# Kernel optimization log

Hardware: AMD Instinct MI355X
Metric: run time of the kernel (lower is better)

The kernel has to match this reference:

```python
import jax, jax.numpy as jnp
import numpy as np

B, S, D = 1, 2048, 2048
H, KVH, HD = 32, 8, 64  # heads, kv heads, head_dim
GROUPS = H // KVH
SCALE = HD ** -0.5


def rotate_half(x):
    x1, x2 = jnp.split(x, 2, axis=-1)
    return jnp.concatenate((-x2, x1), axis=-1)


def setup_inputs() -> dict:
    key = jax.random.key(0)
    ks = jax.random.split(key, 8)
    hidden_states = jax.random.normal(ks[0], (B, S, D), dtype=jnp.float32)
    # RoPE tables: [B, S, HD]
    inv_freq = 1.0 / (10000.0 ** (jnp.arange(0, HD, 2, dtype=jnp.float32) / HD))
    t = jnp.arange(S, dtype=jnp.float32)
    freqs = jnp.outer(t, inv_freq)                      # [S, HD/2]
    emb = jnp.concatenate((freqs, freqs), axis=-1)      # [S, HD]
    cos = jnp.cos(emb)[None]                            # [1, S, HD]
    sin = jnp.sin(emb)[None]
    std = 0.02
    wq = jax.random.normal(ks[1], (H * HD, D), dtype=jnp.float32) * std
    wk = jax.random.normal(ks[2], (KVH * HD, D), dtype=jnp.float32) * std
    wv = jax.random.normal(ks[3], (KVH * HD, D), dtype=jnp.float32) * std
    wo = jax.random.normal(ks[4], (D, H * HD), dtype=jnp.float32) * std
    return {"hidden_states": hidden_states, "cos": cos, "sin": sin,
            "wq": wq, "wk": wk, "wv": wv, "wo": wo}


def reference(hidden_states, cos, sin, wq, wk, wv, wo):
    b, s, d = hidden_states.shape
    # QKV projections (nn.Linear: x @ W.T), split into heads -> [B, H, S, HD]
    q = (hidden_states @ wq.T).reshape(b, s, H, HD).transpose(0, 2, 1, 3)
    k = (hidden_states @ wk.T).reshape(b, s, KVH, HD).transpose(0, 2, 1, 3)
    v = (hidden_states @ wv.T).reshape(b, s, KVH, HD).transpose(0, 2, 1, 3)
    # RoPE (unsqueeze_dim=1)
    c = cos[:, None, :, :]
    sn = sin[:, None, :, :]
    q = q * c + rotate_half(q) * sn
    k = k * c + rotate_half(k) * sn
    # GQA: repeat kv heads to match query heads
    k = jnp.repeat(k, GROUPS, axis=1)
    v = jnp.repeat(v, GROUPS, axis=1)
    # scaled causal softmax attention
    scores = jnp.einsum('bhqd,bhkd->bhqk', q, k) * SCALE
    causal = jnp.tril(jnp.ones((s, s), dtype=bool))
    scores = jnp.where(causal, scores, jnp.finfo(scores.dtype).min)
    probs = jax.nn.softmax(scores, axis=-1)
    attn = jnp.einsum('bhqk,bhkd->bhqd', probs, v)
    attn = attn.transpose(0, 2, 1, 3).reshape(b, s, H * HD)
    return attn @ wo.T
```

## Files before the change

### kernel.cpp

```cpp
#include <hip/hip_runtime.h>
#include <stdint.h>

#define SEQ   2048
#define DMODEL 2048
#define NQH   32
#define NKVH  8
#define HDIM  64
#define QN    (NQH*HDIM)
#define KVNN  (NKVH*HDIM)

typedef __bf16 bf16x8 __attribute__((ext_vector_type(8)));
typedef float  f32x4  __attribute__((ext_vector_type(4)));
typedef unsigned short u16;

__device__ __forceinline__ u16 f2bf(float f) {
  __bf16 h = (__bf16)f;
  return __builtin_bit_cast(u16, h);
}
__device__ __forceinline__ float bf2f(u16 b) {
  return __builtin_bit_cast(float, (uint32_t)b << 16);
}
__device__ __forceinline__ float fexp2(float x) {
#if __has_builtin(__builtin_amdgcn_exp2f)
  return __builtin_amdgcn_exp2f(x);
#else
  return __expf(0.69314718056f * x);
#endif
}
__device__ __forceinline__ bool probe_is_f32(const uint32_t* p) {
  return (p[0] & 0xFFFFu) == 0u;
}

__device__ __forceinline__ void glds16(const u16* g, void* lds) {
  __builtin_amdgcn_global_load_lds(
      (const __attribute__((address_space(1))) uint32_t*)g,
      (__attribute__((address_space(3))) uint32_t*)lds, 16, 0, 0);
}
__device__ __forceinline__ void drain_vm() {
  asm volatile("s_waitcnt vmcnt(0)" ::: "memory");
}

__global__ __launch_bounds__(256)
void conv_all(const void* __restrict__ X, const void* __restrict__ cosv,
              const void* __restrict__ sinv, const void* __restrict__ wq,
              const void* __restrict__ wk, const void* __restrict__ wv,
              const void* __restrict__ wo,
              u16* __restrict__ Xc, u16* __restrict__ cosc, u16* __restrict__ sinc,
              u16* __restrict__ wqc, u16* __restrict__ wkc, u16* __restrict__ wvc,
              u16* __restrict__ woc)
{
  const bool f32in = probe_is_f32((const uint32_t*)cosv);
  const long t = (long)blockIdx.x * 256 + threadIdx.x;
  const void* src; u16* dst; long off;
  if      (t < 524288L)  { src = X;    dst = Xc;   off = t; }
  else if (t < 1048576L) { src = wq;   dst = wqc;  off = t - 524288L; }
  else if (t < 1179648L) { src = wk;   dst = wkc;  off = t - 1048576L; }
  else if (t < 1310720L) { src = wv;   dst = wvc;  off = t - 1179648L; }
  else if (t < 1835008L) { src = wo;   dst = woc;  off = t - 1310720L; }
  else if (t < 1851392L) { src = cosv; dst = cosc; off = t - 1835008L; }
  else                   { src = sinv; dst = sinc; off = t - 1851392L; }
  if (f32in) {
    const float4* s = (const float4*)src;
    float4 a = s[2*off], b = s[2*off + 1];
    union { u16 h[8]; uint4 u; } o;
    o.h[0]=f2bf(a.x); o.h[1]=f2bf(a.y); o.h[2]=f2bf(a.z); o.h[3]=f2bf(a.w);
    o.h[4]=f2bf(b.x); o.h[5]=f2bf(b.y); o.h[6]=f2bf(b.z); o.h[7]=f2bf(b.w);
    *(uint4*)(dst + off*8) = o.u;
  } else {
    *(uint4*)(dst + off*8) = ((const uint4*)src)[off];
  }
}

__global__ __launch_bounds__(256, 4)
void gemm_qkv(const u16* __restrict__ A,
              const u16* __restrict__ wq, const u16* __restrict__ wk,
              const u16* __restrict__ wv,
              u16* __restrict__ Qb, u16* __restrict__ Kb, u16* __restrict__ Vb)
{
  __shared__ __align__(16) u16 As[2][64][32];
  __shared__ __align__(16) u16 Bs[2][128][32];
  const int tid  = threadIdx.x;
  const int wave = tid >> 6;
  const int lane = tid & 63;
  const int quad = lane >> 4;
  const int l16  = lane & 15;
  const int m0 = blockIdx.y * 64;
  const int n0 = blockIdx.x * 128;
  const int wm = (wave & 1) * 32;
  const int wn = (wave >> 1) * 64;
  const int K = DMODEL;
  const int lr = lane >> 2;
  const int lc = (lane & 3) * 8;

  const u16* Bbase; u16* Cbase; int Cstride, nc0;
  if (n0 < 2048)      { Bbase = wq + (size_t)n0 * K;          Cbase = Qb; Cstride = QN;   nc0 = n0; }
  else if (n0 < 2560) { Bbase = wk + (size_t)(n0 - 2048) * K; Cbase = Kb; Cstride = KVNN; nc0 = n0 - 2048; }
  else                { Bbase = wv + (size_t)(n0 - 2560) * K; Cbase = Vb; Cstride = KVNN; nc0 = n0 - 2560; }

  f32x4 acc[2][4];
  #pragma unroll
  for (int i = 0; i < 2; i++)
    #pragma unroll
    for (int j = 0; j < 4; j++)
      acc[i][j] = (f32x4){0.f, 0.f, 0.f, 0.f};

  #define STAGE_QKV(b, k0)                                                        \
    do {                                                                          \
      glds16(A + (size_t)(m0 + 16*wave + lr) * K + (k0) + lc,                     \
             (char*)&As[b][0][0] + wave*1024);                                    \
      glds16(Bbase + (size_t)(16*wave + lr) * K + (k0) + lc,                      \
             (char*)&Bs[b][0][0] + wave*1024);                                    \
      glds16(Bbase + (size_t)(64 + 16*wave + lr) * K + (k0) + lc,                 \
             (char*)&Bs[b][0][0] + (4+wave)*1024);                                \
    } while (0)

  STAGE_QKV(0, 0);
  drain_vm();
  __syncthreads();
  int cur = 0;
  for (int k0 = 0; k0 < K; k0 += 32) {
    if (k0 + 32 < K) STAGE_QKV(cur ^ 1, k0 + 32);
    bf16x8 af[2], bfr[4];
    #pragma unroll
    for (int i = 0; i < 2; i++) af[i]  = *(const bf16x8*)&As[cur][wm + i*16 + l16][quad*8];
    #pragma unroll
    for (int j = 0; j < 4; j++) bfr[j] = *(const bf16x8*)&Bs[cur][wn + j*16 + l16][quad*8];
    #pragma unroll
    for (int i = 0; i < 2; i++)
      #pragma unroll
      for (int j = 0; j < 4; j++)
        acc[i][j] = __builtin_amdgcn_mfma_f32_16x16x32_bf16(af[i], bfr[j], acc[i][j], 0, 0, 0);
    drain_vm();
    __syncthreads();
    cur ^= 1;
  }
  #undef STAGE_QKV

  #pragma unroll
  for (int i = 0; i < 2; i++) {
    const int rb = m0 + wm + i*16 + quad*4;
    #pragma unroll
    for (int j = 0; j < 4; j++) {
      const int col = nc0 + wn + j*16 + l16;
      #pragma unroll
      for (int r = 0; r < 4; r++)
        Cbase[(size_t)(rb + r) * Cstride + col] = f2bf(acc[i][j][r]);
    }
  }
}

__global__ __launch_bounds__(256, 4)
void gemm_nt(const u16* __restrict__ A, const u16* __restrict__ B,
             void* __restrict__ C, int M, int N, int K,
             const uint32_t* outprobe)
{
  __shared__ __align__(16) u16 As[2][64][32];
  __shared__ __align__(16) u16 Bs[2][128][32];
  const int tid  = threadIdx.x;
  const int wave = tid >> 6;
  const int lane = tid & 63;
  const int quad = lane >> 4;
  const int l16  = lane & 15;
  const int m0 = blockIdx.y * 64;
  const int n0 = blockIdx.x * 128;
  const int wm = (wave & 1) * 32;
  const int wn = (wave >> 1) * 64;
  const int lr = lane >> 2;
  const int lc = (lane & 3) * 8;

  f32x4 acc[2][4];
  #pragma unroll
  for (int i = 0; i < 2; i++)
    #pragma unroll
    for (int j = 0; j < 4; j++)
      acc[i][j] = (f32x4){0.f, 0.f, 0.f, 0.f};

  #define STAGE_NT(b, k0)                                                         \
    do {                                                                          \
      glds16(A + (size_t)(m0 + 16*wave + lr) * K + (k0) + lc,                     \
             (char*)&As[b][0][0] + wave*1024);                                    \
      glds16(B + (size_t)(n0 + 16*wave + lr) * K + (k0) + lc,                     \
             (char*)&Bs[b][0][0] + wave*1024);                                    \
      glds16(B + (size_t)(n0 + 64 + 16*wave + lr) * K + (k0) + lc,                \
             (char*)&Bs[b][0][0] + (4+wave)*1024);                                \
    } while (0)

  STAGE_NT(0, 0);
  drain_vm();
  __syncthreads();
  int cur = 0;
  for (int k0 = 0; k0 < K; k0 += 32) {
    if (k0 + 32 < K) STAGE_NT(cur ^ 1, k0 + 32);
    bf16x8 af[2], bfr[4];
    #pragma unroll
    for (int i = 0; i < 2; i++) af[i]  = *(const bf16x8*)&As[cur][wm + i*16 + l16][quad*8];
    #pragma unroll
    for (int j = 0; j < 4; j++) bfr[j] = *(const bf16x8*)&Bs[cur][wn + j*16 + l16][quad*8];
    #pragma unroll
    for (int i = 0; i < 2; i++)
      #pragma unroll
      for (int j = 0; j < 4; j++)
        acc[i][j] = __builtin_amdgcn_mfma_f32_16x16x32_bf16(af[i], bfr[j], acc[i][j], 0, 0, 0);
    drain_vm();
    __syncthreads();
    cur ^= 1;
  }
  #undef STAGE_NT

  const bool f32out = (outprobe != nullptr) && probe_is_f32(outprobe);
  #pragma unroll
  for (int i = 0; i < 2; i++) {
    const int rb = m0 + wm + i*16 + quad*4;
    #pragma unroll
    for (int j = 0; j < 4; j++) {
      const int col = n0 + wn + j*16 + l16;
      if (f32out) {
        float* Cf = (float*)C;
        #pragma unroll
        for (int r = 0; r < 4; r++)
          Cf[(size_t)(rb + r) * N + col] = acc[i][j][r];
      } else {
        u16* Ch = (u16*)C;
        #pragma unroll
        for (int r = 0; r < 4; r++)
          Ch[(size_t)(rb + r) * N + col] = f2bf(acc[i][j][r]);
      }
    }
  }
}

__global__ void rope_k(u16* __restrict__ Kb,
                       const u16* __restrict__ cosb, const u16* __restrict__ sinb)
{
  const int idx = blockIdx.x * 256 + threadIdx.x;
  const int s = idx >> 8;
  const int rem = idx & 255;
  u16* base = Kb + (size_t)s * KVNN + (rem >> 5) * 64;
  const int d = rem & 31;
  const float x1 = bf2f(base[d]);
  const float x2 = bf2f(base[d + 32]);
  const float c  = bf2f(cosb[s * 64 + d]);
  const float sn = bf2f(sinb[s * 64 + d]);
  base[d]      = f2bf(x1 * c - x2 * sn);
  base[d + 32] = f2bf(x2 * c + x1 * sn);
}

__global__ __launch_bounds__(256)
void vtrans(const u16* __restrict__ Vb, u16* __restrict__ Vtg)
{
  __shared__ __align__(16) u16 T[64][72];
  const int tid = threadIdx.x;
  const int hkv = blockIdx.x & 7;
  const int s0  = (blockIdx.x >> 3) * 64;
  const int r = tid >> 3;
  const int c = (tid & 7) * 8;
  *(uint4*)&T[r][c]      = *(const uint4*)(Vb + (size_t)(s0 + r)      * KVNN + hkv*64 + c);
  *(uint4*)&T[r + 32][c] = *(const uint4*)(Vb + (size_t)(s0 + r + 32) * KVNN + hkv*64 + c);
  __syncthreads();
  #pragma unroll
  for (int dd = 0; dd < 64; dd += 32) {
    const int d = (tid >> 3) + dd;
    union { u16 h[8]; uint4 u; } o;
    #pragma unroll
    for (int j = 0; j < 8; j++) o.h[j] = T[c + j][d];
    *(uint4*)(Vtg + (size_t)(hkv*64 + d) * SEQ + s0 + c) = o.u;
  }
}

#define LOG2E 1.4426950408889634f

__device__ __forceinline__ float qmax16(float v) {
  v = fmaxf(v, __shfl_xor(v, 1)); v = fmaxf(v, __shfl_xor(v, 2));
  v = fmaxf(v, __shfl_xor(v, 4)); v = fmaxf(v, __shfl_xor(v, 8));
  return v;
}
__device__ __forceinline__ float qsum16(float v) {
  v += __shfl_xor(v, 1); v += __shfl_xor(v, 2);
  v += __shfl_xor(v, 4); v += __shfl_xor(v, 8);
  return v;
}

__global__ __launch_bounds__(256, 4)
void attn_kernel(const u16* __restrict__ Qb,
                 const u16* __restrict__ Kb,
                 const u16* __restrict__ Vtg,
                 u16* __restrict__ Ob,
                 const u16* __restrict__ cosb, const u16* __restrict__ sinb)
{
  __shared__ __align__(16) u16 Ks[64][72];
  __shared__ __align__(16) u16 Vt[64][72];
  __shared__ __align__(16) u16 Ps[4][16][72];

  const int tid  = threadIdx.x;
  const int wave = tid >> 6;
  const int lane = tid & 63;
  const int quad = lane >> 4;
  const int l16  = lane & 15;
  const int h    = blockIdx.x;
  const int qt   = 31 - blockIdx.y;
  const int hkv  = h >> 2;
  const int qrow0 = qt * 64 + wave * 16;
  const int ktmax = qt + 1;

  bf16x8 qf[2];
  {
    const int qrow = qrow0 + l16;
    const u16* qp = Qb + (size_t)qrow * QN + h*64 + quad*8;
    union { bf16x8 v; u16 h8[8]; } lo, hi, cv, sv, olo, ohi;
    lo.v = *(const bf16x8*)qp;
    hi.v = *(const bf16x8*)(qp + 32);
    cv.v = *(const bf16x8*)(cosb + qrow*64 + quad*8);
    sv.v = *(const bf16x8*)(sinb + qrow*64 + quad*8);
    #pragma unroll
    for (int j = 0; j < 8; j++) {
      const float x1 = bf2f(lo.h8[j]), x2 = bf2f(hi.h8[j]);
      const float c = bf2f(cv.h8[j]), sn = bf2f(sv.h8[j]);
      olo.h8[j] = f2bf((x1*c - x2*sn) * 0.125f);
      ohi.h8[j] = f2bf((x2*c + x1*sn) * 0.125f);
    }
    qf[0] = olo.v;
    qf[1] = ohi.v;
  }

  f32x4 oacc[4];
  #pragma unroll
  for (int nt = 0; nt < 4; nt++) oacc[nt] = (f32x4){0.f, 0.f, 0.f, 0.f};
  float m_run[4], l_run[4];
  #pragma unroll
  for (int r = 0; r < 4; r++) { m_run[r] = -1e30f; l_run[r] = 0.f; }

  const int sr = tid >> 3;
  const int sc = (tid & 7) * 8;

  uint4 k0, k1, v0, v1;
  {
    k0 = *(const uint4*)(Kb + (size_t)(sr)      * KVNN + hkv*64 + sc);
    k1 = *(const uint4*)(Kb + (size_t)(sr + 32) * KVNN + hkv*64 + sc);
    v0 = *(const uint4*)(Vtg + (size_t)(hkv*64 + sr)      * SEQ + sc);
    v1 = *(const uint4*)(Vtg + (size_t)(hkv*64 + sr + 32) * SEQ + sc);
  }

  for (int kt = 0; kt < ktmax; kt++) {
    const int kb = kt * 64;
    const bool diag = (kt == qt);

    __syncthreads();
    *(uint4*)&Ks[sr][sc]      = k0;
    *(uint4*)&Ks[sr + 32][sc] = k1;
    *(uint4*)&Vt[sr][sc]      = v0;
    *(uint4*)&Vt[sr + 32][sc] = v1;
    __syncthreads();

    if (kt + 1 < ktmax) {
      const int kn = kb + 64;
      k0 = *(const uint4*)(Kb + (size_t)(kn + sr)      * KVNN + hkv*64 + sc);
      k1 = *(const uint4*)(Kb + (size_t)(kn + sr + 32) * KVNN + hkv*64 + sc);
      v0 = *(const uint4*)(Vtg + (size_t)(hkv*64 + sr)      * SEQ + kn + sc);
      v1 = *(const uint4*)(Vtg + (size_t)(hkv*64 + sr + 32) * SEQ + kn + sc);
    }

    f32x4 sacc[4];
    #pragma unroll
    for (int nt = 0; nt < 4; nt++) sacc[nt] = (f32x4){0.f, 0.f, 0.f, 0.f};
    #pragma unroll
    for (int ks = 0; ks < 2; ks++)
      #pragma unroll
      for (int nt = 0; nt < 4; nt++)
        if (!diag || nt <= wave) {
          bf16x8 kf = *(const bf16x8*)&Ks[nt*16 + l16][ks*32 + quad*8];
          sacc[nt] = __builtin_amdgcn_mfma_f32_16x16x32_bf16(qf[ks], kf, sacc[nt], 0, 0, 0);
        }
    #pragma unroll
    for (int nt = 0; nt < 4; nt++)
      #pragma unroll
      for (int r = 0; r < 4; r++)
        sacc[nt][r] *= LOG2E;
    if (diag) {
      #pragma unroll
      for (int nt = 0; nt < 4; nt++)
        #pragma unroll
        for (int r = 0; r < 4; r++)
          if (kb + nt*16 + l16 > qrow0 + quad*4 + r)
            sacc[nt][r] = -1e30f;
    }
    float alpha[4];
    #pragma unroll
    for (int r = 0; r < 4; r++) {
      float mx = fmaxf(fmaxf(sacc[0][r], sacc[1][r]), fmaxf(sacc[2][r], sacc[3][r]));
      mx = qmax16(mx);
      const float mnew = fmaxf(m_run[r], mx);
      alpha[r] = fexp2(m_run[r] - mnew);
      m_run[r] = mnew;
      float rs = 0.f;
      #pragma unroll
      for (int nt = 0; nt < 4; nt++) {
        const float p = fexp2(sacc[nt][r] - mnew);
        rs += p;
        Ps[wave][quad*4 + r][nt*16 + l16] = f2bf(p);
      }
      rs = qsum16(rs);
      l_run[r] = l_run[r] * alpha[r] + rs;
    }
    #pragma unroll
    for (int nt = 0; nt < 4; nt++)
      #pragma unroll
      for (int r = 0; r < 4; r++)
        oacc[nt][r] *= alpha[r];
    asm volatile("" ::: "memory");
    #pragma unroll
    for (int ks = 0; ks < 2; ks++) {
      if (diag && wave < 2 && ks == 1) continue;
      bf16x8 pf = *(const bf16x8*)&Ps[wave][l16][ks*32 + quad*8];
      #pragma unroll
      for (int nt = 0; nt < 4; nt++) {
        bf16x8 vf = *(const bf16x8*)&Vt[nt*16 + l16][ks*32 + quad*8];
        oacc[nt] = __builtin_amdgcn_mfma_f32_16x16x32_bf16(pf, vf, oacc[nt], 0, 0, 0);
      }
    }
  }

  #pragma unroll
  for (int r = 0; r < 4; r++) {
    const float inv = 1.0f / l_run[r];
    const int qrow = qrow0 + quad*4 + r;
    #pragma unroll
    for (int nt = 0; nt < 4; nt++)
      Ob[(size_t)qrow * QN + h*64 + nt*16 + l16] = f2bf(oacc[nt][r] * inv);
  }
}

extern "C" void kernel_launch(void* const* d_in, const int* in_sizes, int n_in,
                              void* d_out, int out_size, void* d_ws, size_t ws_size,
                              hipStream_t stream) {
  const void* X    = d_in[0];
  const void* cosr = d_in[1];
  const void* sinr = d_in[2];
  const void* wq   = d_in[3];
  const void* wk   = d_in[4];
  const void* wv   = d_in[5];
  const void* wo   = d_in[6];

  char* ws = (char*)d_ws;
  const size_t MB = 1024u * 1024u;
  u16* Xc   = (u16*)(ws);
  u16* wqc  = (u16*)(ws + 8*MB);
  u16* wkc  = (u16*)(ws + 16*MB);
  u16* wvc  = (u16*)(ws + 18*MB);
  u16* woc  = (u16*)(ws + 20*MB);
  u16* cosc = (u16*)(ws + 28*MB);
  u16* sinc = (u16*)(ws + 28*MB + 256*1024);
  u16* Qb   = (u16*)(ws + 28*MB + 512*1024);
  u16* Kb   = (u16*)(ws + 36*MB + 512*1024);
  u16* Vb   = (u16*)(ws + 38*MB + 512*1024);
  u16* Vtg  = (u16*)(ws + 40*MB + 512*1024);
  u16* Ab   = wqc;

  dim3 blk(256);
  conv_all<<<dim3(7296), blk, 0, stream>>>(X, cosr, sinr, wq, wk, wv, wo,
                                           Xc, cosc, sinc, wqc, wkc, wvc, woc);
  gemm_qkv<<<dim3(24, 32), blk, 0, stream>>>(Xc, wqc, wkc, wvc, Qb, Kb, Vb);
  rope_k<<<dim3((SEQ*NKVH*32)/256), blk, 0, stream>>>(Kb, cosc, sinc);
  vtrans<<<dim3(256), blk, 0, stream>>>(Vb, Vtg);
  attn_kernel<<<dim3(NQH, SEQ/64), blk, 0, stream>>>(Qb, Kb, Vtg, Ab, cosc, sinc);
  gemm_nt<<<dim3(16, 32), blk, 0, stream>>>(Ab, woc, d_out, SEQ, DMODEL, DMODEL,
                                            (const uint32_t*)cosr);
}
```

Measured before the change: 250.7 us.

## Triple-buffer GEMM LDS staging with partial vmcnt waits

Both GEMM kernels (QKV projection and output projection) move from double-buffered to triple-buffered LDS tiles. Two tiles of global-to-LDS loads now stay in flight, and each step waits with s_waitcnt vmcnt(6/3/0) instead of draining all loads, so memory latency overlaps more with MFMA work. The cost is 50% more LDS per block, which may reduce occupancy under launch_bounds(256,4), plus an extra barrier per iteration. The code also relies on the compiler not emitting other vector-memory ops that would throw off the vmcnt counts.

```diff
diff --git a/kernel.cpp b/kernel.cpp
--- a/kernel.cpp
+++ b/kernel.cpp
@@ -36,9 +36,9 @@
       (const __attribute__((address_space(1))) uint32_t*)g,
       (__attribute__((address_space(3))) uint32_t*)lds, 16, 0, 0);
 }
-__device__ __forceinline__ void drain_vm() {
-  asm volatile("s_waitcnt vmcnt(0)" ::: "memory");
-}
+__device__ __forceinline__ void wait_vm6() { asm volatile("s_waitcnt vmcnt(6)" ::: "memory"); }
+__device__ __forceinline__ void wait_vm3() { asm volatile("s_waitcnt vmcnt(3)" ::: "memory"); }
+__device__ __forceinline__ void wait_vm0() { asm volatile("s_waitcnt vmcnt(0)" ::: "memory"); }
 
 __global__ __launch_bounds__(256)
 void conv_all(const void* __restrict__ X, const void* __restrict__ cosv,
@@ -77,8 +77,8 @@
               const u16* __restrict__ wv,
               u16* __restrict__ Qb, u16* __restrict__ Kb, u16* __restrict__ Vb)
 {
-  __shared__ __align__(16) u16 As[2][64][32];
-  __shared__ __align__(16) u16 Bs[2][128][32];
+  __shared__ __align__(16) u16 As[3][64][32];
+  __shared__ __align__(16) u16 Bs[3][128][32];
   const int tid  = threadIdx.x;
   const int wave = tid >> 6;
   const int lane = tid & 63;
@@ -114,12 +114,16 @@
              (char*)&Bs[b][0][0] + (4+wave)*1024);                                \
     } while (0)
 
+  const int NT = K / 32;
   STAGE_QKV(0, 0);
-  drain_vm();
-  __syncthreads();
+  STAGE_QKV(1, 32);
+  STAGE_QKV(2, 64);
   int cur = 0;
-  for (int k0 = 0; k0 < K; k0 += 32) {
-    if (k0 + 32 < K) STAGE_QKV(cur ^ 1, k0 + 32);
+  for (int t = 0; t < NT; ++t) {
+    if      (t < NT - 2) wait_vm6();
+    else if (t == NT - 2) wait_vm3();
+    else                  wait_vm0();
+    __syncthreads();
     bf16x8 af[2], bfr[4];
     #pragma unroll
     for (int i = 0; i < 2; i++) af[i]  = *(const bf16x8*)&As[cur][wm + i*16 + l16][quad*8];
@@ -130,9 +134,9 @@
       #pragma unroll
       for (int j = 0; j < 4; j++)
         acc[i][j] = __builtin_amdgcn_mfma_f32_16x16x32_bf16(af[i], bfr[j], acc[i][j], 0, 0, 0);
-    drain_vm();
-    __syncthreads();
-    cur ^= 1;
+    __syncthreads();
+    if (t + 3 < NT) STAGE_QKV(cur, (t + 3) * 32);
+    cur = (cur == 2) ? 0 : cur + 1;
   }
   #undef STAGE_QKV
 
@@ -154,8 +158,8 @@
              void* __restrict__ C, int M, int N, int K,
              const uint32_t* outprobe)
 {
-  __shared__ __align__(16) u16 As[2][64][32];
-  __shared__ __align__(16) u16 Bs[2][128][32];
+  __shared__ __align__(16) u16 As[3][64][32];
+  __shared__ __align__(16) u16 Bs[3][128][32];
   const int tid  = threadIdx.x;
   const int wave = tid >> 6;
   const int lane = tid & 63;
@@ -185,12 +189,16 @@
              (char*)&Bs[b][0][0] + (4+wave)*1024);                                \
     } while (0)
 
+  const int NT = K / 32;
   STAGE_NT(0, 0);
-  drain_vm();
-  __syncthreads();
+  STAGE_NT(1, 32);
+  STAGE_NT(2, 64);
   int cur = 0;
-  for (int k0 = 0; k0 < K; k0 += 32) {
-    if (k0 + 32 < K) STAGE_NT(cur ^ 1, k0 + 32);
+  for (int t = 0; t < NT; ++t) {
+    if      (t < NT - 2) wait_vm6();
+    else if (t == NT - 2) wait_vm3();
+    else                  wait_vm0();
+    __syncthreads();
     bf16x8 af[2], bfr[4];
     #pragma unroll
     for (int i = 0; i < 2; i++) af[i]  = *(const bf16x8*)&As[cur][wm + i*16 + l16][quad*8];
@@ -201,9 +209,9 @@
       #pragma unroll
       for (int j = 0; j < 4; j++)
         acc[i][j] = __builtin_amdgcn_mfma_f32_16x16x32_bf16(af[i], bfr[j], acc[i][j], 0, 0, 0);
-    drain_vm();
-    __syncthreads();
-    cur ^= 1;
+    __syncthreads();
+    if (t + 3 < NT) STAGE_NT(cur, (t + 3) * 32);
+    cur = (cur == 2) ? 0 : cur + 1;
   }
   #undef STAGE_NT
 
```

After: 252.5 us. No clear change (+0.7%).
